# Kernel optimization log

Measured on AMD Instinct MI355X. Metric: run time of the kernel, lower is better.

The kernel has to match this reference:

```python
import jax, jax.numpy as jnp
import numpy as np

B, L, D = 4, 2048, 1024
NUM_HEADS = 1
HEAD_DIM = D // NUM_HEADS  # 1024


def setup_inputs() -> dict:
    key = jax.random.key(0)
    ks = jax.random.split(key, 12)
    s = 1.0 / np.sqrt(D)
    return {
        "query": jax.random.normal(ks[0], (B, L, D), jnp.float32),
        "key": jax.random.normal(ks[1], (B, L, D), jnp.float32),
        "value": jax.random.normal(ks[2], (B, L, D), jnp.float32),
        "mask": jax.random.randint(ks[3], (B, 1, L, L), 0, 2, jnp.int32),
        "Wq": jax.random.uniform(ks[4], (D, D * NUM_HEADS), jnp.float32, -s, s),
        "bq": jnp.zeros((D * NUM_HEADS,), jnp.float32),
        "Wk": jax.random.uniform(ks[5], (D, D * NUM_HEADS), jnp.float32, -s, s),
        "bk": jnp.zeros((D * NUM_HEADS,), jnp.float32),
        "Wv": jax.random.uniform(ks[6], (D, D * NUM_HEADS), jnp.float32, -s, s),
        "bv": jnp.zeros((D * NUM_HEADS,), jnp.float32),
        "Wo": jax.random.uniform(ks[7], (D * NUM_HEADS, D), jnp.float32, -s, s),
        "bo": jnp.zeros((D,), jnp.float32),
    }


def reference(query, key, value, mask, Wq, bq, Wk, bk, Wv, bv, Wo, bo):
    b, lq = query.shape[0], query.shape[1]
    lk = key.shape[1]
    # project and split heads: (B, L, H, Dh) -> (B, H, L, Dh)
    Q = (query @ Wq + bq).reshape(b, lq, NUM_HEADS, HEAD_DIM).transpose(0, 2, 1, 3)
    K = (key @ Wk + bk).reshape(b, lk, NUM_HEADS, HEAD_DIM).transpose(0, 2, 1, 3)
    V = (value @ Wv + bv).reshape(b, lk, NUM_HEADS, HEAD_DIM).transpose(0, 2, 1, 3)
    scale = 1.0 / jnp.sqrt(jnp.float32(HEAD_DIM))
    scores = jnp.einsum("bhqd,bhkd->bhqk", Q, K) * scale  # (B,H,Lq,Lk)
    scores = jnp.where(mask == 0, jnp.float32(-1e20), scores)
    attn = jax.nn.softmax(scores, axis=-1)
    out = jnp.einsum("bhqk,bhkd->bhqd", attn, V)  # (B,H,Lq,Dh)
    out = out.transpose(0, 2, 1, 3).reshape(b, lq, NUM_HEADS * HEAD_DIM)
    return out @ Wo + bo
```

## Files before the change

### kernel.cpp

```cpp
#include <hip/hip_runtime.h>

#define B_ 4
#define L_ 2048
#define D_ 1024
#define M_FLAT (B_*L_)

typedef unsigned short bf16_t;
typedef __attribute__((ext_vector_type(8))) short bf16x8;
typedef __attribute__((ext_vector_type(4))) float f32x4;

__device__ __forceinline__ bf16_t f2bf(float f) {
  union { float f; unsigned int u; } c; c.f = f;
  unsigned int u = c.u;
  unsigned int r = (u + 0x7fffu + ((u >> 16) & 1u)) >> 16;
  return (bf16_t)r;
}
__device__ __forceinline__ float bf2f(bf16_t h) {
  union { unsigned int u; float f; } c; c.u = ((unsigned int)h) << 16;
  return c.f;
}

__device__ __forceinline__ void gload_lds16(const bf16_t* g, bf16_t* l) {
  __builtin_amdgcn_global_load_lds(
      (const __attribute__((address_space(1))) unsigned int*)g,
      (__attribute__((address_space(3))) unsigned int*)l, 16, 0, 0);
}

#define BARRIER() do { asm volatile("" ::: "memory"); \
                       __builtin_amdgcn_s_barrier();  \
                       asm volatile("" ::: "memory"); } while (0)

__global__ __launch_bounds__(256) void cvt_bf16(const float* __restrict__ in,
                                                bf16_t* __restrict__ out) {
  size_t i = (size_t)blockIdx.x * 256 + threadIdx.x;
  const float4* p = (const float4*)in + i * 2;
  float4 a = p[0], b = p[1];
  union { bf16_t h[8]; uint4 u; } r;
  r.h[0] = f2bf(a.x); r.h[1] = f2bf(a.y); r.h[2] = f2bf(a.z); r.h[3] = f2bf(a.w);
  r.h[4] = f2bf(b.x); r.h[5] = f2bf(b.y); r.h[6] = f2bf(b.z); r.h[7] = f2bf(b.w);
  ((uint4*)out)[i] = r.u;
}

__global__ __launch_bounds__(256) void transpose_cvt(const float* __restrict__ Wsrc,
                                                     bf16_t* __restrict__ Wt) {
  __shared__ float t[32][33];
  int c0 = blockIdx.x * 32, r0 = blockIdx.y * 32;
  int tx = threadIdx.x, ty = threadIdx.y;
#pragma unroll
  for (int i = 0; i < 4; i++)
    t[ty + i * 8][tx] = Wsrc[(size_t)(r0 + ty + i * 8) * D_ + c0 + tx];
  __syncthreads();
#pragma unroll
  for (int i = 0; i < 4; i++)
    Wt[(size_t)(c0 + ty + i * 8) * D_ + r0 + tx] = f2bf(t[tx][ty + i * 8]);
}

__global__ __launch_bounds__(256) void transpose_bf16(const bf16_t* __restrict__ in,
                                                      bf16_t* __restrict__ out,
                                                      int R, int C, long strIn, long strOut) {
  __shared__ bf16_t t[32][33];
  int c0 = blockIdx.x * 32, r0 = blockIdx.y * 32;
  int tx = threadIdx.x, ty = threadIdx.y;
  const bf16_t* ip = in + (size_t)blockIdx.z * strIn;
  bf16_t* op = out + (size_t)blockIdx.z * strOut;
#pragma unroll
  for (int i = 0; i < 4; i++)
    t[ty + i * 8][tx] = ip[(size_t)(r0 + ty + i * 8) * C + c0 + tx];
  __syncthreads();
#pragma unroll
  for (int i = 0; i < 4; i++)
    op[(size_t)(c0 + ty + i * 8) * R + r0 + tx] = t[tx][ty + i * 8];
}

__global__ __launch_bounds__(256) void c2_kernel(const float* __restrict__ bv,
                                                 const float* __restrict__ Wo,
                                                 float* __restrict__ c2) {
  int j = blockIdx.x * 256 + threadIdx.x;
  float s = 0.f;
  for (int k = 0; k < D_; k++) s += bv[k] * Wo[(size_t)k * D_ + j];
  c2[j] = s;
}

__global__ __launch_bounds__(256) void softmax_row(bf16_t* __restrict__ S,
                                                   const int* __restrict__ mask,
                                                   float* __restrict__ rs) {
  int row = blockIdx.x;
  int tid = threadIdx.x;
  uint4* p = (uint4*)(S + (size_t)row * L_);
  const int4* mp = (const int4*)(mask + (size_t)row * L_) + tid * 2;
  int4 m0 = mp[0], m1 = mp[1];
  union { uint4 u; bf16_t h[8]; } v;
  v.u = p[tid];
  int mk[8] = {m0.x, m0.y, m0.z, m0.w, m1.x, m1.y, m1.z, m1.w};
  float sum = 0.f;
#pragma unroll
  for (int j = 0; j < 8; j++) {
    float e = (mk[j] != 0) ? __expf(bf2f(v.h[j])) : 0.0f;
    bf16_t eb = f2bf(e);
    v.h[j] = eb;
    sum += bf2f(eb);
  }
  p[tid] = v.u;
#pragma unroll
  for (int off = 32; off; off >>= 1) sum += __shfl_down(sum, off, 64);
  __shared__ float wsum[4];
  if ((tid & 63) == 0) wsum[tid >> 6] = sum;
  __syncthreads();
  if (tid == 0) rs[row] = fmaxf(wsum[0] + wsum[1] + wsum[2] + wsum[3], 1e-30f);
}

#define MODE_PROJ 0
#define MODE_BF16 1
#define MODE_FIN  2

template <int BM, int MODE>
__global__ __launch_bounds__(512, 2)
void g8(const bf16_t* __restrict__ Abase, int lda, long strA,
        const bf16_t* __restrict__ Bbase, int ldb, long strB,
        void* __restrict__ outp, long strO, int ldo,
        const float* __restrict__ x0, const float* __restrict__ x1,
        const float* __restrict__ x2, int K) {
  constexpr int WROWS = BM / 2;
  constexpr int QAF   = WROWS / 32;
  constexpr int MFR   = WROWS / 16;
  constexpr int AL    = BM / 128;
  constexpr int BL    = 2;
  constexpr int AHB   = WROWS * 128;
  constexpr int BUFB  = (BM + 256) * 128;
  extern __shared__ __align__(16) char smem[];

  const int tid = threadIdx.x, lane = tid & 63, w = tid >> 6;
  const int wm = w >> 2, wn = w & 3;
  const int fr = lane & 15, fs = lane >> 4;
  const int z = blockIdx.z;

  int gx = gridDim.x, nxy = gx * gridDim.y;
  int lin = blockIdx.y * gx + blockIdx.x;
  if ((nxy & 7) == 0) { int q = nxy >> 3; lin = (lin & 7) * q + (lin >> 3); }
  const int mbase = (lin / gx) * BM, nbase = (lin % gx) * 256;

  const bf16_t* A  = Abase + (size_t)z * strA;
  const bf16_t* Bt = Bbase + (size_t)z * strB;

  int offA[2][2], offB[2][2];
#pragma unroll
  for (int h = 0; h < 2; h++)
#pragma unroll
    for (int i = 0; i < 2; i++) {
      int c = i * 512 + tid, row = c >> 3;
      int sg = (c & 7) ^ (row & 7);
      if (i < AL) offA[h][i] = (mbase + h * WROWS + row) * lda + sg * 8;
      offB[h][i] = (nbase + h * 128 + row) * ldb + sg * 8;
    }

  const int swz0 = (fs ^ (fr & 7)) * 16;
  const int swz1 = ((4 + fs) ^ (fr & 7)) * 16;

  bf16x8 af[QAF][2], bfv[2][2][2];
  f32x4 acc[MFR][4] = {};

#define STAGE_A(h, kt, bsel) do {                                             \
    char* hb_ = smem + (bsel) * BUFB + (h) * AHB;                             \
    _Pragma("unroll")                                                         \
    for (int i_ = 0; i_ < AL; ++i_)                                           \
      gload_lds16(A + offA[h][i_] + (kt) * 64,                                \
                  (bf16_t*)(hb_ + (i_ * 512 + tid) * 16));                    \
  } while (0)
#define STAGE_B(h, kt, bsel) do {                                             \
    char* hb_ = smem + (bsel) * BUFB + BM * 128 + (h) * 16384;                \
    _Pragma("unroll")                                                         \
    for (int i_ = 0; i_ < BL; ++i_)                                           \
      gload_lds16(Bt + offB[h][i_] + (kt) * 64,                               \
                  (bf16_t*)(hb_ + (i_ * 512 + tid) * 16));                    \
  } while (0)
#define LOAD_A(bsel, mh) do {                                                 \
    const char* ab_ = smem + (bsel) * BUFB + (wm * WROWS) * 128;              \
    _Pragma("unroll")                                                         \
    for (int i_ = 0; i_ < QAF; ++i_) {                                        \
      int rb_ = ((mh) * (WROWS / 2) + i_ * 16 + fr) * 128;                    \
      af[i_][0] = *(const bf16x8*)(ab_ + rb_ + swz0);                         \
      af[i_][1] = *(const bf16x8*)(ab_ + rb_ + swz1);                         \
    }                                                                         \
  } while (0)
#define LOAD_B(bsel, nh) do {                                                 \
    const char* bb_ = smem + (bsel) * BUFB + BM * 128 + (wn * 64) * 128;      \
    _Pragma("unroll")                                                         \
    for (int j_ = 0; j_ < 2; ++j_) {                                          \
      int rb_ = ((nh) * 32 + j_ * 16 + fr) * 128;                             \
      bfv[nh][j_][0] = *(const bf16x8*)(bb_ + rb_ + swz0);                    \
      bfv[nh][j_][1] = *(const bf16x8*)(bb_ + rb_ + swz1);                    \
    }                                                                         \
  } while (0)
#define MFMA_Q(mh, nh) do {                                                   \
    __builtin_amdgcn_s_setprio(1);                                            \
    _Pragma("unroll")                                                         \
    for (int i_ = 0; i_ < QAF; ++i_)                                          \
    _Pragma("unroll")                                                         \
    for (int j_ = 0; j_ < 2; ++j_) {                                          \
      acc[(mh)*QAF + i_][(nh)*2 + j_] = __builtin_amdgcn_mfma_f32_16x16x32_bf16( \
          af[i_][0], bfv[nh][j_][0], acc[(mh)*QAF + i_][(nh)*2 + j_], 0, 0, 0);  \
      acc[(mh)*QAF + i_][(nh)*2 + j_] = __builtin_amdgcn_mfma_f32_16x16x32_bf16( \
          af[i_][1], bfv[nh][j_][1], acc[(mh)*QAF + i_][(nh)*2 + j_], 0, 0, 0);  \
    }                                                                         \
    __builtin_amdgcn_s_setprio(0);                                            \
  } while (0)
#define LGKM0() do { asm volatile("s_waitcnt lgkmcnt(0)" ::: "memory");       \
                     __builtin_amdgcn_sched_barrier(0); } while (0)
#define VMW() do {                                                            \
    if constexpr (AL == 2) asm volatile("s_waitcnt vmcnt(8)" ::: "memory");   \
    else                   asm volatile("s_waitcnt vmcnt(6)" ::: "memory");   \
  } while (0)

  const int NK = K >> 6, NI = NK >> 1;

  STAGE_B(0, 0, 0); STAGE_B(1, 0, 0); STAGE_A(0, 0, 0); STAGE_A(1, 0, 0);
  STAGE_B(0, 1, 1); STAGE_B(1, 1, 1); STAGE_A(0, 1, 1); STAGE_A(1, 1, 1);
  VMW(); BARRIER();

  for (int it = 0; it < NI; ++it) {
    const int ta = (2 * it + 2 < NK) ? 2 * it + 2 : NK - 1;
    const int tb = (2 * it + 3 < NK) ? 2 * it + 3 : NK - 1;
    LOAD_A(0, 0); LOAD_B(0, 0);
    BARRIER(); LGKM0(); MFMA_Q(0, 0); BARRIER();
    LOAD_B(0, 1);
    BARRIER(); LGKM0(); MFMA_Q(0, 1); BARRIER();
    LOAD_A(0, 1);
    STAGE_B(0, ta, 0); STAGE_B(1, ta, 0);
    BARRIER(); LGKM0(); MFMA_Q(1, 1); BARRIER();
    STAGE_A(0, ta, 0); STAGE_A(1, ta, 0);
    VMW();
    BARRIER(); MFMA_Q(1, 0); BARRIER();
    LOAD_A(1, 0); LOAD_B(1, 0);
    BARRIER(); LGKM0(); MFMA_Q(0, 0); BARRIER();
    LOAD_B(1, 1);
    BARRIER(); LGKM0(); MFMA_Q(0, 1); BARRIER();
    LOAD_A(1, 1);
    STAGE_B(0, tb, 1); STAGE_B(1, tb, 1);
    BARRIER(); LGKM0(); MFMA_Q(1, 1); BARRIER();
    STAGE_A(0, tb, 1); STAGE_A(1, tb, 1);
    VMW();
    BARRIER(); MFMA_Q(1, 0); BARRIER();
  }
  asm volatile("s_waitcnt vmcnt(0)" ::: "memory");

  const int r0 = mbase + wm * WROWS;
  const int c0 = nbase + wn * 64;

  if constexpr (MODE == MODE_PROJ || MODE == MODE_BF16) {
    BARRIER();
    char* ep = smem + w * AHB;
    bf16_t* o = (bf16_t*)outp + (size_t)z * strO;
    const float* bias = nullptr;
    float scale = 1.0f;
    if constexpr (MODE == MODE_PROJ) {
      bias = (z == 0) ? x0 : (z == 1) ? x1 : x2;
      scale = (z == 0) ? 0.03125f : 1.0f;
    }
#pragma unroll
    for (int nf = 0; nf < 4; ++nf) {
      float bv = 0.0f;
      if constexpr (MODE == MODE_PROJ) bv = bias[c0 + nf * 16 + fr];
#pragma unroll
      for (int mf = 0; mf < MFR; ++mf)
#pragma unroll
        for (int jj = 0; jj < 4; ++jj) {
          int row = mf * 16 + fs * 4 + jj;
          int slot = (nf * 2 + (fr >> 3)) ^ ((row >> 1) & 7);
          *(bf16_t*)(ep + row * 128 + slot * 16 + (fr & 7) * 2) =
              f2bf((acc[mf][nf][jj] + bv) * scale);
        }
    }
    const int rl = lane >> 3, sl = lane & 7;
#pragma unroll
    for (int i = 0; i < WROWS / 8; ++i) {
      int row = i * 8 + rl;
      int slot = sl ^ ((row >> 1) & 7);
      uint4 v = *(const uint4*)(ep + row * 128 + slot * 16);
      *(uint4*)&o[(size_t)(r0 + row) * ldo + c0 + sl * 8] = v;
    }
  } else {
    float* o = (float*)outp + (size_t)z * strO;
    const float* rs = x0 + (size_t)z * L_;
#pragma unroll
    for (int mf = 0; mf < MFR; ++mf) {
#pragma unroll
      for (int jj = 0; jj < 4; ++jj) {
        int r = r0 + mf * 16 + fs * 4 + jj;
        float inv = 1.0f / rs[r];
#pragma unroll
        for (int nf = 0; nf < 4; ++nf) {
          int c = c0 + nf * 16 + fr;
          o[(size_t)r * ldo + c] = acc[mf][nf][jj] * inv + x1[c];
        }
      }
    }
  }
#undef STAGE_A
#undef STAGE_B
#undef LOAD_A
#undef LOAD_B
#undef MFMA_Q
#undef LGKM0
#undef VMW
}

extern "C" void kernel_launch(void* const* d_in, const int* in_sizes, int n_in,
                              void* d_out, int out_size, void* d_ws, size_t ws_size,
                              hipStream_t stream) {
  const float* query = (const float*)d_in[0];
  const float* keyi  = (const float*)d_in[1];
  const float* value = (const float*)d_in[2];
  const int*   mask  = (const int*)d_in[3];
  const float* Wq = (const float*)d_in[4];
  const float* bq = (const float*)d_in[5];
  const float* Wk = (const float*)d_in[6];
  const float* bk = (const float*)d_in[7];
  const float* Wv = (const float*)d_in[8];
  const float* bv = (const float*)d_in[9];
  const float* Wo = (const float*)d_in[10];
  const float* bo = (const float*)d_in[11];

  bf16_t* ws = (bf16_t*)d_ws;
  const size_t NE = (size_t)M_FLAT * D_;
  const size_t WE = (size_t)D_ * D_;
  bf16_t* XQ   = ws;
  bf16_t* XK   = ws + NE;
  bf16_t* XV   = ws + 2 * NE;
  bf16_t* WQT  = ws + 3 * NE;
  bf16_t* WKT  = WQT + WE;
  bf16_t* W2T  = WKT + WE;
  bf16_t* WOT  = W2T + WE;
  bf16_t* WVb  = WOT + WE;
  bf16_t* Qb   = WVb + WE;
  bf16_t* Kb   = Qb + NE;
  bf16_t* VW   = Kb + NE;
  bf16_t* W2tmp= VW + NE;
  float*  rsump= (float*)(W2tmp + WE);
  float*  c2p  = rsump + (size_t)B_ * L_;
  bf16_t* Sb   = ws;
  bf16_t* VWt  = XV;

  hipFuncSetAttribute((const void*)g8<256, MODE_PROJ>,
                      hipFuncAttributeMaxDynamicSharedMemorySize, 131072);
  hipFuncSetAttribute((const void*)g8<256, MODE_BF16>,
                      hipFuncAttributeMaxDynamicSharedMemorySize, 131072);
  hipFuncSetAttribute((const void*)g8<128, MODE_BF16>,
                      hipFuncAttributeMaxDynamicSharedMemorySize, 98304);
  hipFuncSetAttribute((const void*)g8<128, MODE_FIN>,
                      hipFuncAttributeMaxDynamicSharedMemorySize, 98304);

  cvt_bf16<<<dim3(4096), dim3(256), 0, stream>>>(query, XQ);
  cvt_bf16<<<dim3(4096), dim3(256), 0, stream>>>(keyi, XK);
  cvt_bf16<<<dim3(4096), dim3(256), 0, stream>>>(value, XV);
  cvt_bf16<<<dim3(512), dim3(256), 0, stream>>>(Wv, WVb);
  transpose_cvt<<<dim3(32, 32), dim3(32, 8), 0, stream>>>(Wq, WQT);
  transpose_cvt<<<dim3(32, 32), dim3(32, 8), 0, stream>>>(Wk, WKT);
  transpose_cvt<<<dim3(32, 32), dim3(32, 8), 0, stream>>>(Wo, WOT);
  c2_kernel<<<dim3(4), dim3(256), 0, stream>>>(bv, Wo, c2p);
  g8<128, MODE_BF16><<<dim3(4, 8, 1), 512, 98304, stream>>>(
      WVb, D_, 0, WOT, D_, 0, W2tmp, 0, D_,
      nullptr, nullptr, nullptr, D_);
  transpose_bf16<<<dim3(32, 32, 1), dim3(32, 8), 0, stream>>>(
      W2tmp, W2T, D_, D_, 0, 0);
  g8<256, MODE_PROJ><<<dim3(4, 32, 3), 512, 131072, stream>>>(
      XQ, D_, (long)NE, WQT, D_, (long)WE, Qb, (long)NE, D_,
      bq, bk, c2p, D_);
  transpose_bf16<<<dim3(32, 64, 4), dim3(32, 8), 0, stream>>>(
      VW, VWt, L_, D_, (long)L_ * D_, (long)D_ * L_);
  g8<256, MODE_BF16><<<dim3(8, 8, 4), 512, 131072, stream>>>(
      Qb, D_, (long)L_ * D_, Kb, D_, (long)L_ * D_, Sb, (long)L_ * L_, L_,
      nullptr, nullptr, nullptr, D_);
  softmax_row<<<dim3(B_ * L_), dim3(256), 0, stream>>>(Sb, mask, rsump);
  g8<128, MODE_FIN><<<dim3(4, 16, 4), 512, 98304, stream>>>(
      Sb, L_, (long)L_ * L_, VWt, L_, (long)D_ * L_, d_out, (long)L_ * D_, D_,
      rsump, bo, nullptr, L_);
}
```

Measured before the change: 262.5 us.

## Fuse masked exp and partial row sums into score GEMM epilogue with bitpacked mask

Removes the separate softmax pass over the bf16 score matrix by applying the mask and exp in the QK^T GEMM epilogue and writing per-tile partial row sums, which a small kernel then reduces. The int32 mask is first packed into 64-bit bitmasks so the epilogue reads 32x less mask data. Block index remapping is also changed to a mode-specific swizzle for L2 locality. This saves a full read and write of the 64MB score matrix, but the pack kernel still has to read the full int32 mask once.

```diff
diff --git a/kernel.cpp b/kernel.cpp
--- a/kernel.cpp
+++ b/kernel.cpp
@@ -81,37 +81,27 @@
   c2[j] = s;
 }
 
-__global__ __launch_bounds__(256) void softmax_row(bf16_t* __restrict__ S,
-                                                   const int* __restrict__ mask,
+__global__ __launch_bounds__(256) void pack_mask(const int* __restrict__ mask,
+                                                 unsigned long long* __restrict__ bm) {
+  size_t gid = (size_t)blockIdx.x * 256 + threadIdx.x;
+  int mi = mask[gid];
+  unsigned long long b = __ballot(mi != 0);
+  if ((threadIdx.x & 63) == 0) bm[gid >> 6] = b;
+}
+
+__global__ __launch_bounds__(256) void reduce_rsum(const float* __restrict__ rsp,
                                                    float* __restrict__ rs) {
-  int row = blockIdx.x;
-  int tid = threadIdx.x;
-  uint4* p = (uint4*)(S + (size_t)row * L_);
-  const int4* mp = (const int4*)(mask + (size_t)row * L_) + tid * 2;
-  int4 m0 = mp[0], m1 = mp[1];
-  union { uint4 u; bf16_t h[8]; } v;
-  v.u = p[tid];
-  int mk[8] = {m0.x, m0.y, m0.z, m0.w, m1.x, m1.y, m1.z, m1.w};
-  float sum = 0.f;
-#pragma unroll
-  for (int j = 0; j < 8; j++) {
-    float e = (mk[j] != 0) ? __expf(bf2f(v.h[j])) : 0.0f;
-    bf16_t eb = f2bf(e);
-    v.h[j] = eb;
-    sum += bf2f(eb);
-  }
-  p[tid] = v.u;
-#pragma unroll
-  for (int off = 32; off; off >>= 1) sum += __shfl_down(sum, off, 64);
-  __shared__ float wsum[4];
-  if ((tid & 63) == 0) wsum[tid >> 6] = sum;
-  __syncthreads();
-  if (tid == 0) rs[row] = fmaxf(wsum[0] + wsum[1] + wsum[2] + wsum[3], 1e-30f);
+  int r = blockIdx.x * 256 + threadIdx.x;
+  float s = 0.f;
+#pragma unroll
+  for (int j = 0; j < 32; j++) s += rsp[(size_t)r * 32 + j];
+  rs[r] = fmaxf(s, 1e-30f);
 }
 
 #define MODE_PROJ 0
 #define MODE_BF16 1
-#define MODE_FIN  2
+#define MODE_S    2
+#define MODE_FIN  3
 
 template <int BM, int MODE>
 __global__ __launch_bounds__(512, 2)
@@ -119,7 +109,9 @@
         const bf16_t* __restrict__ Bbase, int ldb, long strB,
         void* __restrict__ outp, long strO, int ldo,
         const float* __restrict__ x0, const float* __restrict__ x1,
-        const float* __restrict__ x2, int K) {
+        const float* __restrict__ x2,
+        const void* __restrict__ auxp, float* __restrict__ rsp,
+        int K) {
   constexpr int WROWS = BM / 2;
   constexpr int QAF   = WROWS / 32;
   constexpr int MFR   = WROWS / 16;
@@ -130,14 +122,25 @@
   extern __shared__ __align__(16) char smem[];
 
   const int tid = threadIdx.x, lane = tid & 63, w = tid >> 6;
-  const int wm = w >> 2, wn = w & 3;
+  const int wm = w >> 1 >> 1, wn = w & 3;
   const int fr = lane & 15, fs = lane >> 4;
-  const int z = blockIdx.z;
-
-  int gx = gridDim.x, nxy = gx * gridDim.y;
-  int lin = blockIdx.y * gx + blockIdx.x;
-  if ((nxy & 7) == 0) { int q = nxy >> 3; lin = (lin & 7) * q + (lin >> 3); }
-  const int mbase = (lin / gx) * BM, nbase = (lin % gx) * 256;
+
+  int xb, yb, zb;
+  {
+    int f0 = blockIdx.x + gridDim.x * (blockIdx.y + gridDim.y * blockIdx.z);
+    int g = f0 & 7, s = f0 >> 3;
+    if constexpr (MODE == MODE_PROJ) {
+      xb = s & 3; int p = g + 8 * (s >> 2); yb = p & 31; zb = p >> 5;
+    } else if constexpr (MODE == MODE_S) {
+      xb = s & 7; int p = g + 8 * (s >> 3); yb = p & 7;  zb = p >> 3;
+    } else if constexpr (MODE == MODE_FIN) {
+      xb = s & 3; int p = g + 8 * (s >> 2); yb = p & 15; zb = p >> 4;
+    } else {
+      xb = blockIdx.x; yb = blockIdx.y; zb = blockIdx.z;
+    }
+  }
+  const int z = zb;
+  const int mbase = yb * BM, nbase = xb * 256;
 
   const bf16_t* A  = Abase + (size_t)z * strA;
   const bf16_t* Bt = Bbase + (size_t)z * strB;
@@ -278,6 +281,43 @@
       uint4 v = *(const uint4*)(ep + row * 128 + slot * 16);
       *(uint4*)&o[(size_t)(r0 + row) * ldo + c0 + sl * 8] = v;
     }
+  } else if constexpr (MODE == MODE_S) {
+    BARRIER();
+    char* ep = smem + w * AHB;
+    bf16_t* o = (bf16_t*)outp + (size_t)z * strO;
+    const unsigned long long* bw =
+        (const unsigned long long*)auxp +
+        ((size_t)z * L_ + r0) * 32 + (c0 >> 6);
+#pragma unroll
+    for (int mf = 0; mf < MFR; ++mf) {
+#pragma unroll
+      for (int jj = 0; jj < 4; ++jj) {
+        int row = mf * 16 + fs * 4 + jj;
+        unsigned long long wd = bw[(size_t)row * 32];
+        float psum = 0.f;
+#pragma unroll
+        for (int nf = 0; nf < 4; ++nf) {
+          int cbit = nf * 16 + fr;
+          float e = ((wd >> cbit) & 1ull) ? __expf(acc[mf][nf][jj]) : 0.0f;
+          bf16_t eb = f2bf(e);
+          psum += bf2f(eb);
+          int slot = (nf * 2 + (fr >> 3)) ^ ((row >> 1) & 7);
+          *(bf16_t*)(ep + row * 128 + slot * 16 + (fr & 7) * 2) = eb;
+        }
+#pragma unroll
+        for (int off = 8; off; off >>= 1) psum += __shfl_xor(psum, off, 16);
+        if (fr == 0)
+          rsp[((size_t)z * L_ + r0 + row) * 32 + xb * 4 + wn] = psum;
+      }
+    }
+    const int rl = lane >> 3, sl = lane & 7;
+#pragma unroll
+    for (int i = 0; i < WROWS / 8; ++i) {
+      int row = i * 8 + rl;
+      int slot = sl ^ ((row >> 1) & 7);
+      uint4 v = *(const uint4*)(ep + row * 128 + slot * 16);
+      *(uint4*)&o[(size_t)(r0 + row) * ldo + c0 + sl * 8] = v;
+    }
   } else {
     float* o = (float*)outp + (size_t)z * strO;
     const float* rs = x0 + (size_t)z * L_;
@@ -337,18 +377,22 @@
   bf16_t* W2tmp= VW + NE;
   float*  rsump= (float*)(W2tmp + WE);
   float*  c2p  = rsump + (size_t)B_ * L_;
+  float*  rspart = c2p + D_;
+  unsigned long long* bmask =
+      (unsigned long long*)(rspart + (size_t)B_ * L_ * 32);
   bf16_t* Sb   = ws;
   bf16_t* VWt  = XV;
 
   hipFuncSetAttribute((const void*)g8<256, MODE_PROJ>,
                       hipFuncAttributeMaxDynamicSharedMemorySize, 131072);
-  hipFuncSetAttribute((const void*)g8<256, MODE_BF16>,
+  hipFuncSetAttribute((const void*)g8<256, MODE_S>,
                       hipFuncAttributeMaxDynamicSharedMemorySize, 131072);
   hipFuncSetAttribute((const void*)g8<128, MODE_BF16>,
                       hipFuncAttributeMaxDynamicSharedMemorySize, 98304);
   hipFuncSetAttribute((const void*)g8<128, MODE_FIN>,
                       hipFuncAttributeMaxDynamicSharedMemorySize, 98304);
 
+  pack_mask<<<dim3(65536), dim3(256), 0, stream>>>(mask, bmask);
   cvt_bf16<<<dim3(4096), dim3(256), 0, stream>>>(query, XQ);
   cvt_bf16<<<dim3(4096), dim3(256), 0, stream>>>(keyi, XK);
   cvt_bf16<<<dim3(4096), dim3(256), 0, stream>>>(value, XV);
@@ -359,19 +403,19 @@
   c2_kernel<<<dim3(4), dim3(256), 0, stream>>>(bv, Wo, c2p);
   g8<128, MODE_BF16><<<dim3(4, 8, 1), 512, 98304, stream>>>(
       WVb, D_, 0, WOT, D_, 0, W2tmp, 0, D_,
-      nullptr, nullptr, nullptr, D_);
+      nullptr, nullptr, nullptr, nullptr, nullptr, D_);
   transpose_bf16<<<dim3(32, 32, 1), dim3(32, 8), 0, stream>>>(
       W2tmp, W2T, D_, D_, 0, 0);
   g8<256, MODE_PROJ><<<dim3(4, 32, 3), 512, 131072, stream>>>(
       XQ, D_, (long)NE, WQT, D_, (long)WE, Qb, (long)NE, D_,
-      bq, bk, c2p, D_);
+      bq, bk, c2p, nullptr, nullptr, D_);
   transpose_bf16<<<dim3(32, 64, 4), dim3(32, 8), 0, stream>>>(
       VW, VWt, L_, D_, (long)L_ * D_, (long)D_ * L_);
-  g8<256, MODE_BF16><<<dim3(8, 8, 4), 512, 131072, stream>>>(
+  g8<256, MODE_S><<<dim3(8, 8, 4), 512, 131072, stream>>>(
       Qb, D_, (long)L_ * D_, Kb, D_, (long)L_ * D_, Sb, (long)L_ * L_, L_,
-      nullptr, nullptr, nullptr, D_);
-  softmax_row<<<dim3(B_ * L_), dim3(256), 0, stream>>>(Sb, mask, rsump);
+      nullptr, nullptr, nullptr, bmask, rspart, D_);
+  reduce_rsum<<<dim3(32), dim3(256), 0, stream>>>(rspart, rsump);
   g8<128, MODE_FIN><<<dim3(4, 16, 4), 512, 98304, stream>>>(
       Sb, L_, (long)L_ * L_, VWt, L_, (long)D_ * L_, d_out, (long)L_ * D_, D_,
-      rsump, bo, nullptr, L_);
-}
+      rsump, bo, nullptr, nullptr, nullptr, L_);
+}
```

After: 299.9 us. 1.14x slower.
